# Kernel tuning notes

Measured on AMD Instinct MI355X. Metric: run time of the kernel, lower is better.

Reference implementation:

```python
import jax, jax.numpy as jnp
import numpy as np

B, N, D, H = 32, 128, 64, 128


def setup_inputs() -> dict:
    key = jax.random.key(0)
    ks = jax.random.split(key, 16)
    s = 0.05
    inp = {
        "x": jax.random.normal(ks[0], (B, N, D), dtype=jnp.float32),
        "masks": jax.random.randint(ks[1], (B, N), 0, 2, dtype=jnp.int32),
        # message_net: Linear(2D,H) -> ReLU -> Linear(H,H)
        "W1": jax.random.normal(ks[2], (2 * D, H), dtype=jnp.float32) * s,
        "b1": jax.random.normal(ks[3], (H,), dtype=jnp.float32) * s,
        "W2": jax.random.normal(ks[4], (H, H), dtype=jnp.float32) * s,
        "b2": jax.random.normal(ks[5], (H,), dtype=jnp.float32) * s,
        # attention_net: Linear(2D,H) -> ReLU -> Linear(H,1)
        "A1": jax.random.normal(ks[6], (2 * D, H), dtype=jnp.float32) * s,
        "ab1": jax.random.normal(ks[7], (H,), dtype=jnp.float32) * s,
        "A2": jax.random.normal(ks[8], (H, 1), dtype=jnp.float32) * s,
        "ab2": jax.random.normal(ks[9], (1,), dtype=jnp.float32) * s,
        # update_net: Linear(D+H,H) -> ReLU -> Linear(H,D)
        "U1": jax.random.normal(ks[10], (D + H, H), dtype=jnp.float32) * s,
        "ub1": jax.random.normal(ks[11], (H,), dtype=jnp.float32) * s,
        "U2": jax.random.normal(ks[12], (H, D), dtype=jnp.float32) * s,
        "ub2": jax.random.normal(ks[13], (D,), dtype=jnp.float32) * s,
    }
    return inp


def reference(x, masks, W1, b1, W2, b2, A1, ab1, A2, ab2, U1, ub1, U2, ub2):
    d = x.shape[-1]
    # pairs = cat([x_i, x_j]); Linear(pairs) == x_i @ W[:d] + x_j @ W[d:] + b
    # message MLP hidden: (B, N, N, H)
    h = jax.nn.relu(
        jnp.einsum("bid,dh->bih", x, W1[:d])[:, :, None, :]
        + jnp.einsum("bjd,dh->bjh", x, W1[d:])[:, None, :, :]
        + b1
    )
    messages = jnp.einsum("bijh,hk->bijk", h, W2) + b2  # (B, N, N, H)
    # attention MLP
    ha = jax.nn.relu(
        jnp.einsum("bid,dh->bih", x, A1[:d])[:, :, None, :]
        + jnp.einsum("bjd,dh->bjh", x, A1[d:])[:, None, :, :]
        + ab1
    )
    logits = jnp.einsum("bijh,h->bij", ha, A2[:, 0]) + ab2[0]  # (B, N, N)
    m = masks.astype(bool)[:, None, :]  # mask over j (source agents)
    logits = jnp.where(m, logits, -jnp.inf)
    attn = jax.nn.softmax(logits, axis=-1)
    attn = jnp.where(m, attn, 0.0)
    agg = jnp.einsum("bijh,bij->bih", messages, attn)  # (B, N, H)
    comb = jnp.concatenate([x, agg], axis=-1)  # (B, N, D+H)
    upd = jax.nn.relu(comb @ U1 + ub1) @ U2 + ub2  # (B, N, D)
    return x + upd
```

## Files before the change

### kernel.cpp

```cpp
#include <hip/hip_runtime.h>
#include <hip/hip_bf16.h>
#include <stdint.h>

#define NN 128
#define DD 64
#define HH 128

__device__ __forceinline__ float bflo(uint32_t u){ union{uint32_t u;float f;} c; c.u = u<<16; return c.f; }
__device__ __forceinline__ float bfhi(uint32_t u){ union{uint32_t u;float f;} c; c.u = u & 0xffff0000u; return c.f; }
__device__ __forceinline__ uint32_t packbf(float lo, float hi){
  __hip_bfloat16 a = __float2bfloat16(lo);
  __hip_bfloat16 b = __float2bfloat16(hi);
  uint16_t ua = *(uint16_t*)&a, ub = *(uint16_t*)&b;
  return (uint32_t)ua | ((uint32_t)ub<<16);
}

__global__ __launch_bounds__(128) void k1_proj(
    const float* __restrict__ x,
    const float* __restrict__ W1, const float* __restrict__ b1,
    const float* __restrict__ A1, const float* __restrict__ ab1,
    const float* __restrict__ W2, const float* __restrict__ b2,
    const float* __restrict__ U1, const float* __restrict__ ub1,
    float* __restrict__ Pm, float* __restrict__ Pa,
    uint32_t* __restrict__ Qmp, uint32_t* __restrict__ Qap,
    float* __restrict__ M, float* __restrict__ c0){
  const int bid = blockIdx.x;
  const int t = threadIdx.x;
  if(bid >= 512){
    int hb = bid - 512;
    if(hb < HH){
      float acc = 0.f;
      #pragma unroll 4
      for(int k=0;k<HH;k++) acc += W2[hb*HH+k] * U1[(DD+k)*HH+t];
      M[hb*HH+t] = acc;
    } else {
      float acc = ub1[t];
      #pragma unroll 4
      for(int k=0;k<HH;k++) acc += b2[k] * U1[(DD+k)*HH+t];
      c0[t] = acc;
    }
    return;
  }
  const int g = bid & 15, b = bid >> 4;
  const int jb = g*4;
  __shared__ float xs[8][64];
  __shared__ float qmS[8][128];
  __shared__ float qaS[8][128];
  {
    int r = t >> 4, d4 = (t & 15)*4;
    int gr = (r<4) ? (jb+r) : (jb + r - 4 + 64);
    *(float4*)&xs[r][d4] = *(const float4*)&x[(b*NN+gr)*DD + d4];
  }
  __syncthreads();
  float pm[8], qm[8], pa[8], qa[8];
  #pragma unroll
  for(int r=0;r<8;r++){ pm[r]=0.f;qm[r]=0.f;pa[r]=0.f;qa[r]=0.f; }
  for(int d0=0; d0<DD; d0+=4){
    float4 xr[8];
    #pragma unroll
    for(int r=0;r<8;r++) xr[r] = *(const float4*)&xs[r][d0];
    #pragma unroll
    for(int dd=0; dd<4; dd++){
      const int d = d0 + dd;
      float w1a = W1[d*HH + t];
      float w1b = W1[(DD+d)*HH + t];
      float a1a = A1[d*HH + t];
      float a1b = A1[(DD+d)*HH + t];
      #pragma unroll
      for(int r=0;r<8;r++){
        float xv = (&xr[r].x)[dd];
        pm[r] += xv*w1a; qm[r] += xv*w1b;
        pa[r] += xv*a1a; qa[r] += xv*a1b;
      }
    }
  }
  float b1v = b1[t], ab1v = ab1[t];
  #pragma unroll
  for(int r=0;r<8;r++){
    int gr = (r<4) ? (jb+r) : (jb + r - 4 + 64);
    Pm[(b*NN+gr)*HH + t] = pm[r] + b1v;
    Pa[(b*NN+gr)*HH + t] = pa[r] + ab1v;
    qmS[r][t] = qm[r];
    qaS[r][t] = qa[r];
  }
  __syncthreads();
  #pragma unroll
  for(int k=0;k<4;k++){
    int idx = t + k*128;
    int r = idx >> 6, hp = idx & 63;
    int gr = (r<4) ? (jb+r) : (jb + r - 4 + 64);
    Qmp[(b*NN+gr)*64 + hp] = packbf(qmS[r][hp], qmS[r][hp+64]);
    Qap[(b*NN+gr)*64 + hp] = packbf(qaS[r][hp], qaS[r][hp+64]);
  }
}

__global__ __launch_bounds__(256) void k2_attn_hbar(
    const float* __restrict__ Pa, const float* __restrict__ Pm,
    const uint32_t* __restrict__ Qap, const uint32_t* __restrict__ Qmp,
    const float* __restrict__ A2, const int* __restrict__ masks,
    float* __restrict__ hbar){
  const int it = blockIdx.x;
  const int b  = blockIdx.y;
  const int t = threadIdx.x;
  const int wave = t>>6, lane = t&63;
  __shared__ uint32_t qbuf[NN*65];
  __shared__ float pS[8*HH];
  __shared__ float a2S[HH];
  __shared__ float atS[8*NN];
  {
    const uint32_t* src = Qap + (size_t)b*NN*64;
    #pragma unroll
    for(int k=0;k<8;k++){
      int idx4 = t + k*256;
      int j = idx4 >> 4, hp4 = (idx4 & 15)*4;
      uint4 v = *(const uint4*)&src[j*64 + hp4];
      uint32_t* d = &qbuf[j*65 + hp4];
      d[0]=v.x; d[1]=v.y; d[2]=v.z; d[3]=v.w;
    }
    int r = t>>5, h4 = (t&31)*4;
    *(float4*)&pS[r*HH + h4] = *(const float4*)&Pa[(b*NN + it*8 + r)*HH + h4];
    if(t < HH) a2S[t] = A2[t];
  }
  __syncthreads();
  const int i0 = wave*2, i1 = i0+1;
  float a00=0.f,a01=0.f,a10=0.f,a11=0.f;
  for(int h0=0; h0<64; h0+=4){
    float4 p0a = *(const float4*)&pS[i0*HH + h0];
    float4 p0b = *(const float4*)&pS[i0*HH + 64 + h0];
    float4 p1a = *(const float4*)&pS[i1*HH + h0];
    float4 p1b = *(const float4*)&pS[i1*HH + 64 + h0];
    float4 a2a = *(const float4*)&a2S[h0];
    float4 a2b = *(const float4*)&a2S[64 + h0];
    #pragma unroll
    for(int dd=0; dd<4; dd++){
      uint32_t q0 = qbuf[lane*65 + h0 + dd];
      uint32_t q1 = qbuf[(lane+64)*65 + h0 + dd];
      float q0l=bflo(q0), q0h=bfhi(q0), q1l=bflo(q1), q1h=bfhi(q1);
      float pa0=(&p0a.x)[dd], pb0=(&p0b.x)[dd];
      float pa1=(&p1a.x)[dd], pb1=(&p1b.x)[dd];
      float aa=(&a2a.x)[dd],  ab=(&a2b.x)[dd];
      a00 += fmaxf(pa0+q0l,0.f)*aa; a00 += fmaxf(pb0+q0h,0.f)*ab;
      a01 += fmaxf(pa0+q1l,0.f)*aa; a01 += fmaxf(pb0+q1h,0.f)*ab;
      a10 += fmaxf(pa1+q0l,0.f)*aa; a10 += fmaxf(pb1+q0h,0.f)*ab;
      a11 += fmaxf(pa1+q1l,0.f)*aa; a11 += fmaxf(pb1+q1h,0.f)*ab;
    }
  }
  const int m0 = masks[b*NN + lane];
  const int m1 = masks[b*NN + 64 + lane];
  const float NEG = -3.0e38f;
  #pragma unroll
  for(int ii=0; ii<2; ii++){
    float x0 = ii ? a10 : a00, x1 = ii ? a11 : a01;
    int il = ii ? i1 : i0;
    float l0 = m0 ? x0 : NEG, l1 = m1 ? x1 : NEG;
    float v = fmaxf(l0, l1);
    for(int off=32; off>=1; off>>=1) v = fmaxf(v, __shfl_xor(v, off));
    float e0 = m0 ? __expf(x0 - v) : 0.f;
    float e1 = m1 ? __expf(x1 - v) : 0.f;
    float s = e0 + e1;
    for(int off=32; off>=1; off>>=1) s += __shfl_xor(s, off);
    float inv = (s > 0.f) ? (1.f/s) : 0.f;
    atS[il*NN + lane]      = e0*inv;
    atS[il*NN + 64 + lane] = e1*inv;
  }
  __syncthreads();
  {
    const uint32_t* src = Qmp + (size_t)b*NN*64;
    #pragma unroll
    for(int k=0;k<8;k++){
      int idx4 = t + k*256;
      int j = idx4 >> 4, hp4 = (idx4 & 15)*4;
      uint4 v = *(const uint4*)&src[j*64 + hp4];
      uint32_t* d = &qbuf[j*65 + hp4];
      d[0]=v.x; d[1]=v.y; d[2]=v.z; d[3]=v.w;
    }
    int r = t>>5, h4 = (t&31)*4;
    *(float4*)&pS[r*HH + h4] = *(const float4*)&Pm[(b*NN + it*8 + r)*HH + h4];
  }
  __syncthreads();
  float pm00 = pS[i0*HH + lane], pm01 = pS[i0*HH + 64 + lane];
  float pm10 = pS[i1*HH + lane], pm11 = pS[i1*HH + 64 + lane];
  float h00=0.f,h01=0.f,h10=0.f,h11=0.f;
  for(int j0=0; j0<NN; j0+=4){
    float4 at0 = *(const float4*)&atS[i0*NN + j0];
    float4 at1 = *(const float4*)&atS[i1*NN + j0];
    #pragma unroll
    for(int dd=0; dd<4; dd++){
      uint32_t qd = qbuf[(j0+dd)*65 + lane];
      float ql = bflo(qd), qh = bfhi(qd);
      float w0 = (&at0.x)[dd], w1 = (&at1.x)[dd];
      h00 += w0*fmaxf(pm00+ql,0.f);
      h01 += w0*fmaxf(pm01+qh,0.f);
      h10 += w1*fmaxf(pm10+ql,0.f);
      h11 += w1*fmaxf(pm11+qh,0.f);
    }
  }
  const int gi0 = b*NN + it*8 + i0, gi1 = gi0 + 1;
  hbar[gi0*HH + lane]      = h00;
  hbar[gi0*HH + 64 + lane] = h01;
  hbar[gi1*HH + lane]      = h10;
  hbar[gi1*HH + 64 + lane] = h11;
}

__global__ __launch_bounds__(256) void k3_update(
    const float* __restrict__ x, const float* __restrict__ hbar,
    const float* __restrict__ M, const float* __restrict__ c0,
    const float* __restrict__ U1, const float* __restrict__ U2,
    const float* __restrict__ ub2, float* __restrict__ out){
  const int bid = blockIdx.x;
  const int t = threadIdx.x;
  const int r0 = bid*16;
  __shared__ float xs[16][64];
  __shared__ float hb[16][128];
  __shared__ float hidS[16][128];
  __shared__ float c0S[128];
  {
    int r = t>>4, d4 = (t&15)*4;
    *(float4*)&xs[r][d4] = *(const float4*)&x[(r0+r)*DD + d4];
    int r1 = t>>5, h4 = (t&31)*4;
    *(float4*)&hb[r1][h4]   = *(const float4*)&hbar[(r0+r1)*HH + h4];
    *(float4*)&hb[r1+8][h4] = *(const float4*)&hbar[(r0+r1+8)*HH + h4];
    if(t<128) c0S[t] = c0[t];
  }
  __syncthreads();
  {
    const int c = t & 127, g = t>>7;
    float acc[8];
    #pragma unroll
    for(int r=0;r<8;r++) acc[r]=0.f;
    for(int d0=0; d0<DD; d0+=4){
      float4 xr[8];
      #pragma unroll
      for(int r=0;r<8;r++) xr[r] = *(const float4*)&xs[g*8+r][d0];
      #pragma unroll
      for(int dd=0; dd<4; dd++){
        float u = U1[(d0+dd)*HH + c];
        #pragma unroll
        for(int r=0;r<8;r++) acc[r] += (&xr[r].x)[dd]*u;
      }
    }
    for(int h0=0; h0<HH; h0+=4){
      float4 hr[8];
      #pragma unroll
      for(int r=0;r<8;r++) hr[r] = *(const float4*)&hb[g*8+r][h0];
      #pragma unroll
      for(int dd=0; dd<4; dd++){
        float mv = M[(h0+dd)*HH + c];
        #pragma unroll
        for(int r=0;r<8;r++) acc[r] += (&hr[r].x)[dd]*mv;
      }
    }
    float cc = c0S[c];
    #pragma unroll
    for(int r=0;r<8;r++) hidS[g*8+r][c] = fmaxf(acc[r]+cc, 0.f);
  }
  __syncthreads();
  {
    const int dcol = t & 63, rg = t>>6;
    float acc2[4];
    #pragma unroll
    for(int r=0;r<4;r++) acc2[r]=0.f;
    for(int ci=0; ci<HH; ci+=4){
      float4 hr[4];
      #pragma unroll
      for(int r=0;r<4;r++) hr[r] = *(const float4*)&hidS[rg*4+r][ci];
      #pragma unroll
      for(int dd=0; dd<4; dd++){
        float u2 = U2[(ci+dd)*DD + dcol];
        #pragma unroll
        for(int r=0;r<4;r++) acc2[r] += (&hr[r].x)[dd]*u2;
      }
    }
    float ub = ub2[dcol];
    #pragma unroll
    for(int r=0;r<4;r++){
      int row = r0 + rg*4 + r;
      out[row*DD + dcol] = xs[rg*4+r][dcol] + acc2[r] + ub;
    }
  }
}

extern "C" void kernel_launch(void* const* d_in, const int* in_sizes, int n_in,
                              void* d_out, int out_size, void* d_ws, size_t ws_size,
                              hipStream_t stream){
  const float* x   = (const float*)d_in[0];
  const int*   msk = (const int*)d_in[1];
  const float* W1  = (const float*)d_in[2];
  const float* b1  = (const float*)d_in[3];
  const float* W2  = (const float*)d_in[4];
  const float* b2  = (const float*)d_in[5];
  const float* A1  = (const float*)d_in[6];
  const float* ab1 = (const float*)d_in[7];
  const float* A2  = (const float*)d_in[8];
  const float* U1  = (const float*)d_in[10];
  const float* ub1 = (const float*)d_in[11];
  const float* U2  = (const float*)d_in[12];
  const float* ub2 = (const float*)d_in[13];
  float* out = (float*)d_out;

  char* w = (char*)d_ws;
  float*    Pm   = (float*)(w);
  float*    Pa   = (float*)(w + (2u<<20));
  uint32_t* Qmp  = (uint32_t*)(w + (4u<<20));
  uint32_t* Qap  = (uint32_t*)(w + (5u<<20));
  float*    hbar = (float*)(w + (6u<<20));
  float*    M    = (float*)(w + (8u<<20));
  float*    c0   = (float*)(w + (8u<<20) + (64u<<10));

  hipLaunchKernelGGL(k1_proj, dim3(641), dim3(128), 0, stream,
                     x, W1, b1, A1, ab1, W2, b2, U1, ub1,
                     Pm, Pa, Qmp, Qap, M, c0);
  hipLaunchKernelGGL(k2_attn_hbar, dim3(16,32), dim3(256), 0, stream,
                     Pa, Pm, Qap, Qmp, A2, msk, hbar);
  hipLaunchKernelGGL(k3_update, dim3(256), dim3(256), 0, stream,
                     x, hbar, M, c0, U1, U2, ub2, out);
}
```

Baseline: 126.8 us.

## Fuse update MLP into attention kernel, drop hbar round trip

```diff
diff --git a/kernel.cpp b/kernel.cpp
--- a/kernel.cpp
+++ b/kernel.cpp
@@ -94,11 +94,14 @@
   }
 }
 
-__global__ __launch_bounds__(256) void k2_attn_hbar(
+__global__ __launch_bounds__(256) void k2_fused(
     const float* __restrict__ Pa, const float* __restrict__ Pm,
     const uint32_t* __restrict__ Qap, const uint32_t* __restrict__ Qmp,
     const float* __restrict__ A2, const int* __restrict__ masks,
-    float* __restrict__ hbar){
+    const float* __restrict__ x, const float* __restrict__ M,
+    const float* __restrict__ c0,
+    const float* __restrict__ U1, const float* __restrict__ U2,
+    const float* __restrict__ ub2, float* __restrict__ out){
   const int it = blockIdx.x;
   const int b  = blockIdx.y;
   const int t = threadIdx.x;
@@ -107,6 +110,7 @@
   __shared__ float pS[8*HH];
   __shared__ float a2S[HH];
   __shared__ float atS[8*NN];
+  __shared__ float xs[8][DD];
   {
     const uint32_t* src = Qap + (size_t)b*NN*64;
     #pragma unroll
@@ -120,6 +124,10 @@
     int r = t>>5, h4 = (t&31)*4;
     *(float4*)&pS[r*HH + h4] = *(const float4*)&Pa[(b*NN + it*8 + r)*HH + h4];
     if(t < HH) a2S[t] = A2[t];
+    if(t < 128){
+      int xr = t >> 4, d4 = (t & 15)*4;
+      *(float4*)&xs[xr][d4] = *(const float4*)&x[(b*NN + it*8 + xr)*DD + d4];
+    }
   }
   __syncthreads();
   const int i0 = wave*2, i1 = i0+1;
@@ -195,87 +203,64 @@
       h11 += w1*fmaxf(pm11+qh,0.f);
     }
   }
-  const int gi0 = b*NN + it*8 + i0, gi1 = gi0 + 1;
-  hbar[gi0*HH + lane]      = h00;
-  hbar[gi0*HH + 64 + lane] = h01;
-  hbar[gi1*HH + lane]      = h10;
-  hbar[gi1*HH + 64 + lane] = h11;
-}
-
-__global__ __launch_bounds__(256) void k3_update(
-    const float* __restrict__ x, const float* __restrict__ hbar,
-    const float* __restrict__ M, const float* __restrict__ c0,
-    const float* __restrict__ U1, const float* __restrict__ U2,
-    const float* __restrict__ ub2, float* __restrict__ out){
-  const int bid = blockIdx.x;
-  const int t = threadIdx.x;
-  const int r0 = bid*16;
-  __shared__ float xs[16][64];
-  __shared__ float hb[16][128];
-  __shared__ float hidS[16][128];
-  __shared__ float c0S[128];
-  {
-    int r = t>>4, d4 = (t&15)*4;
-    *(float4*)&xs[r][d4] = *(const float4*)&x[(r0+r)*DD + d4];
-    int r1 = t>>5, h4 = (t&31)*4;
-    *(float4*)&hb[r1][h4]   = *(const float4*)&hbar[(r0+r1)*HH + h4];
-    *(float4*)&hb[r1+8][h4] = *(const float4*)&hbar[(r0+r1+8)*HH + h4];
-    if(t<128) c0S[t] = c0[t];
-  }
-  __syncthreads();
-  {
-    const int c = t & 127, g = t>>7;
-    float acc[8];
-    #pragma unroll
-    for(int r=0;r<8;r++) acc[r]=0.f;
+  __syncthreads();
+  pS[i0*HH + lane]      = h00;
+  pS[i0*HH + 64 + lane] = h01;
+  pS[i1*HH + lane]      = h10;
+  pS[i1*HH + 64 + lane] = h11;
+  __syncthreads();
+  {
+    const int c = t & 127, gg = t >> 7;
+    float acc[4];
+    #pragma unroll
+    for(int r=0;r<4;r++) acc[r]=0.f;
     for(int d0=0; d0<DD; d0+=4){
-      float4 xr[8];
-      #pragma unroll
-      for(int r=0;r<8;r++) xr[r] = *(const float4*)&xs[g*8+r][d0];
-      #pragma unroll
-      for(int dd=0; dd<4; dd++){
-        float u = U1[(d0+dd)*HH + c];
-        #pragma unroll
-        for(int r=0;r<8;r++) acc[r] += (&xr[r].x)[dd]*u;
+      float u0 = U1[(d0+0)*HH + c];
+      float u1 = U1[(d0+1)*HH + c];
+      float u2 = U1[(d0+2)*HH + c];
+      float u3 = U1[(d0+3)*HH + c];
+      #pragma unroll
+      for(int r=0;r<4;r++){
+        float4 xv = *(const float4*)&xs[gg*4+r][d0];
+        acc[r] += xv.x*u0 + xv.y*u1 + xv.z*u2 + xv.w*u3;
       }
     }
     for(int h0=0; h0<HH; h0+=4){
-      float4 hr[8];
-      #pragma unroll
-      for(int r=0;r<8;r++) hr[r] = *(const float4*)&hb[g*8+r][h0];
-      #pragma unroll
-      for(int dd=0; dd<4; dd++){
-        float mv = M[(h0+dd)*HH + c];
-        #pragma unroll
-        for(int r=0;r<8;r++) acc[r] += (&hr[r].x)[dd]*mv;
-      }
-    }
-    float cc = c0S[c];
-    #pragma unroll
-    for(int r=0;r<8;r++) hidS[g*8+r][c] = fmaxf(acc[r]+cc, 0.f);
-  }
-  __syncthreads();
-  {
-    const int dcol = t & 63, rg = t>>6;
-    float acc2[4];
-    #pragma unroll
-    for(int r=0;r<4;r++) acc2[r]=0.f;
+      float m0v = M[(h0+0)*HH + c];
+      float m1v = M[(h0+1)*HH + c];
+      float m2v = M[(h0+2)*HH + c];
+      float m3v = M[(h0+3)*HH + c];
+      #pragma unroll
+      for(int r=0;r<4;r++){
+        float4 hv = *(const float4*)&pS[(gg*4+r)*HH + h0];
+        acc[r] += hv.x*m0v + hv.y*m1v + hv.z*m2v + hv.w*m3v;
+      }
+    }
+    float cc = c0[c];
+    #pragma unroll
+    for(int r=0;r<4;r++) atS[(gg*4+r)*NN + c] = fmaxf(acc[r]+cc, 0.f);
+  }
+  __syncthreads();
+  {
+    const int dcol = t & 63, rg = t >> 6;
+    float acc2[2];
+    acc2[0]=0.f; acc2[1]=0.f;
     for(int ci=0; ci<HH; ci+=4){
-      float4 hr[4];
-      #pragma unroll
-      for(int r=0;r<4;r++) hr[r] = *(const float4*)&hidS[rg*4+r][ci];
-      #pragma unroll
-      for(int dd=0; dd<4; dd++){
-        float u2 = U2[(ci+dd)*DD + dcol];
-        #pragma unroll
-        for(int r=0;r<4;r++) acc2[r] += (&hr[r].x)[dd]*u2;
+      float u20 = U2[(ci+0)*DD + dcol];
+      float u21 = U2[(ci+1)*DD + dcol];
+      float u22 = U2[(ci+2)*DD + dcol];
+      float u23 = U2[(ci+3)*DD + dcol];
+      #pragma unroll
+      for(int r=0;r<2;r++){
+        float4 hv = *(const float4*)&atS[(rg*2+r)*NN + ci];
+        acc2[r] += hv.x*u20 + hv.y*u21 + hv.z*u22 + hv.w*u23;
       }
     }
     float ub = ub2[dcol];
     #pragma unroll
-    for(int r=0;r<4;r++){
-      int row = r0 + rg*4 + r;
-      out[row*DD + dcol] = xs[rg*4+r][dcol] + acc2[r] + ub;
+    for(int r=0;r<2;r++){
+      int grow = b*NN + it*8 + rg*2 + r;
+      out[grow*DD + dcol] = xs[rg*2+r][dcol] + acc2[r] + ub;
     }
   }
 }
@@ -303,15 +288,12 @@
   float*    Pa   = (float*)(w + (2u<<20));
   uint32_t* Qmp  = (uint32_t*)(w + (4u<<20));
   uint32_t* Qap  = (uint32_t*)(w + (5u<<20));
-  float*    hbar = (float*)(w + (6u<<20));
   float*    M    = (float*)(w + (8u<<20));
   float*    c0   = (float*)(w + (8u<<20) + (64u<<10));
 
   hipLaunchKernelGGL(k1_proj, dim3(641), dim3(128), 0, stream,
                      x, W1, b1, A1, ab1, W2, b2, U1, ub1,
                      Pm, Pa, Qmp, Qap, M, c0);
-  hipLaunchKernelGGL(k2_attn_hbar, dim3(16,32), dim3(256), 0, stream,
-                     Pa, Pm, Qap, Qmp, A2, msk, hbar);
-  hipLaunchKernelGGL(k3_update, dim3(256), dim3(256), 0, stream,
-                     x, hbar, M, c0, U1, U2, ub2, out);
-}
+  hipLaunchKernelGGL(k2_fused, dim3(16,32), dim3(256), 0, stream,
+                     Pa, Pm, Qap, Qmp, A2, msk, x, M, c0, U1, U2, ub2, out);
+}
```

Result: faster. 117.1 us (-7.7%).
